# Kernel optimization log

Hardware: AMD Instinct MI355X
Metric: run time of the kernel (lower is better)

Reference implementation:

```python
import jax, jax.numpy as jnp
import numpy as np

B, S, F = 4, 2048, 512
H, DH, OUT = 8, 64, 512  # attention_dim=512 -> head_dim=64
NEG_SLOPE = 0.01


def setup_inputs() -> dict:
    key = jax.random.key(0)
    ks = jax.random.split(key, 9)
    sc_in = 1.0 / np.sqrt(F)
    sc_hd = 1.0 / np.sqrt(H * DH)
    return {
        "x": jax.random.normal(ks[0], (B, S, F), dtype=jnp.float32),
        "Wq": jax.random.normal(ks[1], (F, H, DH), dtype=jnp.float32) * sc_in,
        "bq": jnp.zeros((H, DH), dtype=jnp.float32),
        "Wk": jax.random.normal(ks[2], (F, H, DH), dtype=jnp.float32) * sc_in,
        "bk": jnp.zeros((H, DH), dtype=jnp.float32),
        "Wv": jax.random.normal(ks[3], (F, H, DH), dtype=jnp.float32) * sc_in,
        "bv": jnp.zeros((H, DH), dtype=jnp.float32),
        "Wo": jax.random.normal(ks[4], (H, DH, OUT), dtype=jnp.float32) * sc_hd,
        "bo": jnp.zeros((OUT,), dtype=jnp.float32),
    }


def reference(x, Wq, bq, Wk, bk, Wv, bv, Wo, bo):
    # QKV projections: DenseGeneral(axis=-1, features=(H, DH)) -> [B, S, H, DH]
    q = jnp.einsum('bsf,fhd->bshd', x, Wq) + bq
    k = jnp.einsum('bsf,fhd->bshd', x, Wk) + bk
    v = jnp.einsum('bsf,fhd->bshd', x, Wv) + bv

    # Pairwise squared L2: l2[b,h,i,j] = ||q[b,i,h]-k[b,j,h]||^2
    q2 = jnp.sum(q * q, axis=-1)              # [B, S, H]
    k2 = jnp.sum(k * k, axis=-1)              # [B, S, H]
    qk = jnp.einsum('bihd,bjhd->bhij', q, k)  # [B, H, S, S]
    l2 = (q2.transpose(0, 2, 1)[:, :, :, None]
          + k2.transpose(0, 2, 1)[:, :, None, :]
          - 2.0 * qk)

    # softmax over key axis j, then weights.T @ value (note the transpose:
    # output token index is j, summed over query index i, as in the original)
    w = jax.nn.softmax(-l2, axis=-1)                  # [B, H, Si, Sj]
    attn = jnp.einsum('bhij,bihd->bjhd', w, v)        # [B, S, H, DH]

    # out DenseGeneral contracting (H, DH)
    out = jnp.einsum('bshd,hdo->bso', attn, Wo) + bo
    return jnp.where(out >= 0, out, NEG_SLOPE * out)
```

## Files before the change

kernel.cpp:

```cpp
#include <hip/hip_runtime.h>


typedef __attribute__((ext_vector_type(8))) short bf16x8;
typedef __attribute__((ext_vector_type(4))) float f32x4;
typedef __attribute__((ext_vector_type(4))) unsigned short u16x4;

#define MFMA16 __builtin_amdgcn_mfma_f32_16x16x32_bf16
#define LOG2E 1.4426950408889634f
#define TWO_LOG2E 2.8853900817779268f

__device__ inline unsigned short f2bf(float f) {
  unsigned int u = __float_as_uint(f);
  unsigned int r = 0x7fffu + ((u >> 16) & 1u);
  return (unsigned short)((u + r) >> 16);
}
__device__ inline float bf2f(unsigned short h) {
  return __uint_as_float(((unsigned int)h) << 16);
}
__device__ inline float fexp2(float x) { return __builtin_amdgcn_exp2f(x); }

__device__ inline void gl_lds16(const unsigned short* g, unsigned short* lds) {
  __builtin_amdgcn_global_load_lds(
      (const __attribute__((address_space(1))) unsigned int*)g,
      (__attribute__((address_space(3))) unsigned int*)lds, 16, 0, 0);
}

#define NXB4 (8192*512/4)
#define NWQ (1536*512)
#define NWO (512*512)

__global__ __launch_bounds__(256) void prep(
    const float* __restrict__ x, const float* __restrict__ Wq,
    const float* __restrict__ Wk, const float* __restrict__ Wv,
    const float* __restrict__ Wo, const float* __restrict__ bq,
    const float* __restrict__ bk, const float* __restrict__ bv,
    unsigned short* __restrict__ xb, unsigned short* __restrict__ wqkvT,
    unsigned short* __restrict__ woT, float* __restrict__ biasp) {
  int i = blockIdx.x * blockDim.x + threadIdx.x;
  if (i < NXB4) {
    f32x4 v = ((const f32x4*)x)[i];
    u16x4 o;
    o.x = f2bf(v.x); o.y = f2bf(v.y); o.z = f2bf(v.z); o.w = f2bf(v.w);
    ((u16x4*)xb)[i] = o;
    return;
  }
  i -= NXB4;
  if (i < NWQ) {
    int n = i >> 9, f = i & 511;
    const float* W = (n < 512) ? Wq : (n < 1024) ? Wk : Wv;
    wqkvT[i] = f2bf(W[f * 512 + (n & 511)]);
    return;
  }
  i -= NWQ;
  if (i < NWO) {
    int o = i >> 9, hd = i & 511;
    woT[i] = f2bf(Wo[hd * 512 + o]);
    return;
  }
  i -= NWO;
  if (i < 1536) {
    biasp[i] = (i < 512) ? bq[i] : (i < 1024) ? bk[i - 512] : bv[i - 1024];
  }
}

template<int MODE>
__global__ __launch_bounds__(256) void gemm_bt(
    const unsigned short* __restrict__ A, const unsigned short* __restrict__ Bt,
    const float* __restrict__ bias,
    unsigned short* __restrict__ o_q, unsigned short* __restrict__ o_k,
    unsigned short* __restrict__ o_v, float* __restrict__ o_f, int K) {
  const int m0 = blockIdx.y * 128;
  const int n0 = blockIdx.x * 128;
  const int tid = threadIdx.x;
  const int w = tid >> 6, l = tid & 63, lg = l >> 4, ll = l & 15;
  const int wr = w >> 1, wc = w & 1;
  __shared__ unsigned short a_lds[128 * 32];
  __shared__ unsigned short b_lds[128 * 32];
  f32x4 acc[4][4] = {};
  const int nkt = K >> 5;
  for (int kt = 0; kt < nkt; ++kt) {
#pragma unroll
    for (int c = 0; c < 2; ++c) {
      const int cc_base = c * 256 + w * 64;
      const int cc = cc_base + l;
      const int row = cc >> 2, cl = cc & 3;
      gl_lds16(A + (size_t)(m0 + row) * K + kt * 32 + cl * 8, a_lds + cc_base * 8);
      gl_lds16(Bt + (size_t)(n0 + row) * K + kt * 32 + cl * 8, b_lds + cc_base * 8);
    }
    __syncthreads();
    bf16x8 af[4], bfr[4];
#pragma unroll
    for (int mi = 0; mi < 4; ++mi)
      af[mi] = *(const bf16x8*)(a_lds + (wr * 64 + mi * 16 + ll) * 32 + lg * 8);
#pragma unroll
    for (int ni = 0; ni < 4; ++ni)
      bfr[ni] = *(const bf16x8*)(b_lds + (wc * 64 + ni * 16 + ll) * 32 + lg * 8);
#pragma unroll
    for (int mi = 0; mi < 4; ++mi)
#pragma unroll
      for (int ni = 0; ni < 4; ++ni)
        acc[mi][ni] = MFMA16(af[mi], bfr[ni], acc[mi][ni], 0, 0, 0);
    __syncthreads();
  }
#pragma unroll
  for (int mi = 0; mi < 4; ++mi)
#pragma unroll
    for (int ni = 0; ni < 4; ++ni) {
      const int col = n0 + wc * 64 + ni * 16 + ll;
      const float bb = bias[col];
#pragma unroll
      for (int r = 0; r < 4; ++r) {
        const int row = m0 + wr * 64 + mi * 16 + lg * 4 + r;
        float v = acc[mi][ni][r] + bb;
        if (MODE == 0) {
          const int which = col >> 9, h = (col >> 6) & 7, d = col & 63;
          const int b = row >> 11, s = row & 2047;
          if (which == 0) v *= TWO_LOG2E;
          const size_t idx = ((size_t)((b * 8 + h) * 2048 + s)) * 64 + d;
          (which == 0 ? o_q : which == 1 ? o_k : o_v)[idx] = f2bf(v);
        } else {
          v = v >= 0.f ? v : 0.01f * v;
          o_f[(size_t)row * 512 + col] = v;
        }
      }
    }
}

__global__ __launch_bounds__(256) void k2_kernel(const unsigned short* __restrict__ k_g,
                                                 float* __restrict__ k2l_g) {
  const int lane = threadIdx.x & 63;
  const int wid = (blockIdx.x * blockDim.x + threadIdx.x) >> 6;
  const int nw = (gridDim.x * blockDim.x) >> 6;
  for (int row = wid; row < 32 * 2048; row += nw) {
    float v = bf2f(k_g[(size_t)row * 64 + lane]);
    v *= v;
#pragma unroll
    for (int m = 1; m < 64; m <<= 1) v += __shfl_xor(v, m);
    if (lane == 0) k2l_g[row] = LOG2E * v;
  }
}

__global__ __launch_bounds__(256) void transpose_v(const unsigned short* __restrict__ v_g,
                                                   const float* __restrict__ invl_g,
                                                   unsigned short* __restrict__ vt_g) {
  const int bh = blockIdx.x >> 5, st = blockIdx.x & 31;
  const int s0 = st * 64;
  __shared__ unsigned short tile[64][72];
  const int t = threadIdx.x;
  {
    const int sl = t >> 2, cg = t & 3;
    const float sc = invl_g[bh * 2048 + s0 + sl];
    const unsigned short* src = v_g + ((size_t)(bh * 2048 + s0 + sl)) * 64 + cg * 16;
    bf16x8 v0 = *(const bf16x8*)(src);
    bf16x8 v1 = *(const bf16x8*)(src + 8);
#pragma unroll
    for (int e = 0; e < 8; ++e) tile[sl][cg * 16 + e] = f2bf(sc * bf2f((unsigned short)v0[e]));
#pragma unroll
    for (int e = 0; e < 8; ++e) tile[sl][cg * 16 + 8 + e] = f2bf(sc * bf2f((unsigned short)v1[e]));
  }
  __syncthreads();
  {
    const int dl = t >> 2, sg = t & 3;
    bf16x8 o0, o1;
#pragma unroll
    for (int e = 0; e < 8; ++e) o0[e] = (short)tile[sg * 16 + e][dl];
#pragma unroll
    for (int e = 0; e < 8; ++e) o1[e] = (short)tile[sg * 16 + 8 + e][dl];
    unsigned short* dst = vt_g + ((size_t)(bh * 64 + dl)) * 2048 + s0 + sg * 16;
    *(bf16x8*)dst = o0;
    *(bf16x8*)(dst + 8) = o1;
  }
}

__global__ __launch_bounds__(256) void pass1(const unsigned short* __restrict__ q_g,
                                             const unsigned short* __restrict__ k_g,
                                             const float* __restrict__ k2l_g,
                                             float* __restrict__ invl_g) {
  const int bx = blockIdx.x;
  const int bh = (bx & 7) * 4 + ((bx >> 3) >> 4);
  const int ib = (bx >> 3) & 15;
  const int i0 = ib * 128;
  const int tid = threadIdx.x, w = tid >> 6, l = tid & 63, lg = l >> 4, ll = l & 15;
  __shared__ unsigned short k_lds[64 * 64];
  __shared__ float k2_lds[64];
  const unsigned short* qrow = q_g + ((size_t)(bh * 2048 + i0 + w * 32 + ll)) * 64;
  const bf16x8 qa00 = *(const bf16x8*)(qrow + lg * 8);
  const bf16x8 qa01 = *(const bf16x8*)(qrow + 32 + lg * 8);
  const bf16x8 qa10 = *(const bf16x8*)(qrow + 1024 + lg * 8);
  const bf16x8 qa11 = *(const bf16x8*)(qrow + 1024 + 32 + lg * 8);
  float lrun0[4] = {0.f, 0.f, 0.f, 0.f};
  float lrun1[4] = {0.f, 0.f, 0.f, 0.f};
  for (int jt = 0; jt < 32; ++jt) {
    const int j0 = jt * 64;
#pragma unroll
    for (int c = 0; c < 2; ++c) {
      const int cc_base = c * 256 + w * 64;
      const int cc = cc_base + l;
      const int row = cc >> 3, cl = cc & 7;
      gl_lds16(k_g + ((size_t)(bh * 2048 + j0 + row)) * 64 + ((cl ^ (row & 7)) * 8),
               k_lds + cc_base * 8);
    }
    if (tid < 64) k2_lds[tid] = k2l_g[bh * 2048 + j0 + tid];
    __syncthreads();
#pragma unroll
    for (int nf = 0; nf < 4; ++nf) {
      const int jr = nf * 16 + ll;
      const unsigned short* kb = k_lds + jr * 64;
      const int sw = jr & 7;
      bf16x8 b0 = *(const bf16x8*)(kb + ((lg ^ sw) * 8));
      bf16x8 b1 = *(const bf16x8*)(kb + (((4 + lg) ^ sw) * 8));
      f32x4 sa0 = {};
      sa0 = MFMA16(qa00, b0, sa0, 0, 0, 0);
      sa0 = MFMA16(qa01, b1, sa0, 0, 0, 0);
      f32x4 sa1 = {};
      sa1 = MFMA16(qa10, b0, sa1, 0, 0, 0);
      sa1 = MFMA16(qa11, b1, sa1, 0, 0, 0);
      const float k2v = k2_lds[jr];
      lrun0[0] += fexp2(sa0[0] - k2v);
      lrun0[1] += fexp2(sa0[1] - k2v);
      lrun0[2] += fexp2(sa0[2] - k2v);
      lrun0[3] += fexp2(sa0[3] - k2v);
      lrun1[0] += fexp2(sa1[0] - k2v);
      lrun1[1] += fexp2(sa1[1] - k2v);
      lrun1[2] += fexp2(sa1[2] - k2v);
      lrun1[3] += fexp2(sa1[3] - k2v);
    }
    __syncthreads();
  }
#pragma unroll
  for (int r = 0; r < 4; ++r) {
    float t0 = lrun0[r], t1 = lrun1[r];
#pragma unroll
    for (int m = 1; m < 16; m <<= 1) { t0 += __shfl_xor(t0, m); t1 += __shfl_xor(t1, m); }
    if (ll == 0) {
      invl_g[bh * 2048 + i0 + w * 32 + lg * 4 + r] = 1.f / t0;
      invl_g[bh * 2048 + i0 + w * 32 + 16 + lg * 4 + r] = 1.f / t1;
    }
  }
}

__global__ __launch_bounds__(256) void pass2(const unsigned short* __restrict__ q_g,
                                             const unsigned short* __restrict__ k_g,
                                             const unsigned short* __restrict__ vt_g,
                                             const float* __restrict__ k2l_g,
                                             unsigned short* __restrict__ part0,
                                             unsigned short* __restrict__ part1,
                                             unsigned short* __restrict__ part2) {
  const int bx = blockIdx.x;
  const int bh = (bx & 7) * 4 + ((bx >> 3) >> 4);
  const int jb = (bx >> 3) & 15;
  const int by = blockIdx.y;
  const int j0 = jb * 128;
  const int it0 = by * 11;
  const int it_end = (by == 2) ? 32 : it0 + 11;
  const int tid = threadIdx.x, w = tid >> 6, l = tid & 63, lg = l >> 4, ll = l & 15;
  __shared__ unsigned short q_lds[2][64 * 64];
  __shared__ unsigned short vt_lds[2][64 * 64];
  __shared__ unsigned short p_lds[128 * 64];
  const unsigned short* q_base = q_g + (size_t)bh * 2048 * 64;
  const unsigned short* vt_base = vt_g + (size_t)bh * 64 * 2048;
  const unsigned short* krow = k_g + ((size_t)(bh * 2048 + j0 + w * 32 + ll)) * 64;
  const bf16x8 ka00 = *(const bf16x8*)(krow + lg * 8);
  const bf16x8 ka01 = *(const bf16x8*)(krow + 32 + lg * 8);
  const bf16x8 ka10 = *(const bf16x8*)(krow + 1024 + lg * 8);
  const bf16x8 ka11 = *(const bf16x8*)(krow + 1024 + 32 + lg * 8);
  float k2v0[4], k2v1[4];
#pragma unroll
  for (int r = 0; r < 4; ++r) {
    k2v0[r] = k2l_g[bh * 2048 + j0 + w * 32 + lg * 4 + r];
    k2v1[r] = k2l_g[bh * 2048 + j0 + w * 32 + 16 + lg * 4 + r];
  }
  f32x4 oacc0[4] = {};
  f32x4 oacc1[4] = {};
  const int pslot = it0 & 1;
#pragma unroll
  for (int c = 0; c < 2; ++c) {
    const int cc_base = c * 256 + w * 64;
    const int cc = cc_base + l;
    const int row = cc >> 3, cl = cc & 7;
    const int csw = (cl ^ (row & 7)) * 8;
    gl_lds16(q_base + (size_t)(it0 * 64 + row) * 64 + csw, &q_lds[pslot][cc_base * 8]);
    gl_lds16(vt_base + (size_t)row * 2048 + it0 * 64 + csw, &vt_lds[pslot][cc_base * 8]);
  }
  __syncthreads();
  for (int it = it0; it < it_end; ++it) {
    const int slot = it & 1;
    if (it + 1 < it_end) {
      const int i1 = (it + 1) * 64;
#pragma unroll
      for (int c = 0; c < 2; ++c) {
        const int cc_base = c * 256 + w * 64;
        const int cc = cc_base + l;
        const int row = cc >> 3, cl = cc & 7;
        const int csw = (cl ^ (row & 7)) * 8;
        gl_lds16(q_base + (size_t)(i1 + row) * 64 + csw, &q_lds[slot ^ 1][cc_base * 8]);
        gl_lds16(vt_base + (size_t)row * 2048 + i1 + csw, &vt_lds[slot ^ 1][cc_base * 8]);
      }
    }
#pragma unroll
    for (int nf = 0; nf < 4; ++nf) {
      const int ir = nf * 16 + ll;
      const unsigned short* qb = &q_lds[slot][ir * 64];
      const int sw = ir & 7;
      bf16x8 b0 = *(const bf16x8*)(qb + ((lg ^ sw) * 8));
      bf16x8 b1 = *(const bf16x8*)(qb + (((4 + lg) ^ sw) * 8));
      f32x4 sa0 = {};
      sa0 = MFMA16(ka00, b0, sa0, 0, 0, 0);
      sa0 = MFMA16(ka01, b1, sa0, 0, 0, 0);
      f32x4 sa1 = {};
      sa1 = MFMA16(ka10, b0, sa1, 0, 0, 0);
      sa1 = MFMA16(ka11, b1, sa1, 0, 0, 0);
#pragma unroll
      for (int r = 0; r < 4; ++r) {
        const float p0 = fexp2(sa0[r] - k2v0[r]);
        const float p1 = fexp2(sa1[r] - k2v1[r]);
        const int ja = w * 32 + lg * 4 + r;
        const int jb2 = ja + 16;
        p_lds[ja * 64 + (ir ^ ((ja & 7) << 3))] =
            (unsigned short)(__float_as_uint(p0) >> 16);
        p_lds[jb2 * 64 + (ir ^ ((jb2 & 7) << 3))] =
            (unsigned short)(__float_as_uint(p1) >> 16);
      }
    }
    {
      const int jr0 = w * 32 + ll;
      const int jr1 = jr0 + 16;
      const int swp = ll & 7;
      const unsigned short* pb0 = p_lds + jr0 * 64;
      const unsigned short* pb1 = p_lds + jr1 * 64;
      bf16x8 pa00 = *(const bf16x8*)(pb0 + ((lg ^ swp) * 8));
      bf16x8 pa01 = *(const bf16x8*)(pb0 + (((4 + lg) ^ swp) * 8));
      bf16x8 pa10 = *(const bf16x8*)(pb1 + ((lg ^ swp) * 8));
      bf16x8 pa11 = *(const bf16x8*)(pb1 + (((4 + lg) ^ swp) * 8));
#pragma unroll
      for (int nf = 0; nf < 4; ++nf) {
        const int dr = nf * 16 + ll;
        const unsigned short* vb = &vt_lds[slot][dr * 64];
        const int sw = dr & 7;
        bf16x8 v0 = *(const bf16x8*)(vb + ((lg ^ sw) * 8));
        bf16x8 v1 = *(const bf16x8*)(vb + (((4 + lg) ^ sw) * 8));
        oacc0[nf] = MFMA16(pa00, v0, oacc0[nf], 0, 0, 0);
        oacc0[nf] = MFMA16(pa01, v1, oacc0[nf], 0, 0, 0);
        oacc1[nf] = MFMA16(pa10, v0, oacc1[nf], 0, 0, 0);
        oacc1[nf] = MFMA16(pa11, v1, oacc1[nf], 0, 0, 0);
      }
    }
    __syncthreads();
  }
  unsigned short* po = (by == 0) ? part0 : (by == 1) ? part1 : part2;
  const int b = bh >> 3, h2 = bh & 7;
#pragma unroll
  for (int nf = 0; nf < 4; ++nf) {
    const int d = nf * 16 + ll;
#pragma unroll
    for (int r = 0; r < 4; ++r) {
      const int j = j0 + w * 32 + lg * 4 + r;
      po[((size_t)(b * 2048 + j)) * 512 + h2 * 64 + d] = f2bf(oacc0[nf][r]);
      po[((size_t)(b * 2048 + j + 16)) * 512 + h2 * 64 + d] = f2bf(oacc1[nf][r]);
    }
  }
}

__global__ __launch_bounds__(256) void combine3(unsigned short* __restrict__ p0,
                                                const unsigned short* __restrict__ p1,
                                                const unsigned short* __restrict__ p2) {
  const int i = blockIdx.x * blockDim.x + threadIdx.x;
  bf16x8 a = ((const bf16x8*)p0)[i];
  bf16x8 b = ((const bf16x8*)p1)[i];
  bf16x8 c = ((const bf16x8*)p2)[i];
  bf16x8 o;
#pragma unroll
  for (int e = 0; e < 8; ++e)
    o[e] = (short)f2bf(bf2f((unsigned short)a[e]) + bf2f((unsigned short)b[e]) +
                       bf2f((unsigned short)c[e]));
  ((bf16x8*)p0)[i] = o;
}

extern "C" void kernel_launch(void* const* d_in, const int* in_sizes, int n_in,
                              void* d_out, int out_size, void* d_ws, size_t ws_size,
                              hipStream_t stream) {
  const float* x  = (const float*)d_in[0];
  const float* Wq = (const float*)d_in[1];
  const float* bq = (const float*)d_in[2];
  const float* Wk = (const float*)d_in[3];
  const float* bk = (const float*)d_in[4];
  const float* Wv = (const float*)d_in[5];
  const float* bv = (const float*)d_in[6];
  const float* Wo = (const float*)d_in[7];
  const float* bo = (const float*)d_in[8];
  float* out = (float*)d_out;
  char* ws = (char*)d_ws;

  unsigned short* xb    = (unsigned short*)(ws);
  unsigned short* wqkvT = (unsigned short*)(ws + 8388608);
  unsigned short* woT   = (unsigned short*)(ws + 9961472);
  float*          biasp = (float*)         (ws + 10485760);
  unsigned short* q_g   = (unsigned short*)(ws + 10493952);
  unsigned short* k_g   = (unsigned short*)(ws + 18882560);
  unsigned short* v_g   = (unsigned short*)(ws + 27271168);
  unsigned short* vt_g  = (unsigned short*)(ws + 35659776);
  float*          k2_g  = (float*)         (ws + 44048384);
  float*          invl_g= (float*)         (ws + 44310528);
  unsigned short* attnb = (unsigned short*)(ws + 44572672);
  if (ws_size < (size_t)52961280) return;

  prep<<<8199, 256, 0, stream>>>(x, Wq, Wk, Wv, Wo, bq, bk, bv, xb, wqkvT, woT, biasp);
  gemm_bt<0><<<dim3(12, 64), 256, 0, stream>>>(xb, wqkvT, biasp, q_g, k_g, v_g, nullptr, 512);
  k2_kernel<<<1024, 256, 0, stream>>>(k_g, k2_g);
  pass1<<<512, 256, 0, stream>>>(q_g, k_g, k2_g, invl_g);
  transpose_v<<<1024, 256, 0, stream>>>(v_g, invl_g, vt_g);
  pass2<<<dim3(512, 3), 256, 0, stream>>>(q_g, k_g, vt_g, k2_g, attnb, xb, v_g);
  combine3<<<2048, 256, 0, stream>>>(attnb, xb, v_g);
  gemm_bt<1><<<dim3(4, 64), 256, 0, stream>>>(attnb, woT, bo, nullptr, nullptr, nullptr, out, 512);
}
```

Baseline: 159.3 us.

## Tile weight transposes, remap GEMM block order, double-buffer K in pass1

Weight transpose-and-convert moves out of the elementwise prep kernel into a separate packW kernel that transposes through a padded 64x65 shared-memory tile, so both reads and writes are coalesced. The GEMM maps its linear block id with a stride-8 permutation, which changes which output tiles run together, likely to improve L2 reuse. Pass1 double-buffers the K tile and k2 values in LDS so the next tile's loads are issued while the current tile computes. The costs are one extra kernel launch and twice the LDS in pass1.

```diff
diff --git a/kernel.cpp b/kernel.cpp
--- a/kernel.cpp
+++ b/kernel.cpp
@@ -26,16 +26,11 @@
 }
 
 #define NXB4 (8192*512/4)
-#define NWQ (1536*512)
-#define NWO (512*512)
 
 __global__ __launch_bounds__(256) void prep(
-    const float* __restrict__ x, const float* __restrict__ Wq,
-    const float* __restrict__ Wk, const float* __restrict__ Wv,
-    const float* __restrict__ Wo, const float* __restrict__ bq,
+    const float* __restrict__ x, const float* __restrict__ bq,
     const float* __restrict__ bk, const float* __restrict__ bv,
-    unsigned short* __restrict__ xb, unsigned short* __restrict__ wqkvT,
-    unsigned short* __restrict__ woT, float* __restrict__ biasp) {
+    unsigned short* __restrict__ xb, float* __restrict__ biasp) {
   int i = blockIdx.x * blockDim.x + threadIdx.x;
   if (i < NXB4) {
     f32x4 v = ((const f32x4*)x)[i];
@@ -45,21 +40,36 @@
     return;
   }
   i -= NXB4;
-  if (i < NWQ) {
-    int n = i >> 9, f = i & 511;
-    const float* W = (n < 512) ? Wq : (n < 1024) ? Wk : Wv;
-    wqkvT[i] = f2bf(W[f * 512 + (n & 511)]);
-    return;
-  }
-  i -= NWQ;
-  if (i < NWO) {
-    int o = i >> 9, hd = i & 511;
-    woT[i] = f2bf(Wo[hd * 512 + o]);
-    return;
-  }
-  i -= NWO;
   if (i < 1536) {
     biasp[i] = (i < 512) ? bq[i] : (i < 1024) ? bk[i - 512] : bv[i - 1024];
+  }
+}
+
+__global__ __launch_bounds__(256) void packW(
+    const float* __restrict__ Wq, const float* __restrict__ Wk,
+    const float* __restrict__ Wv, const float* __restrict__ Wo,
+    unsigned short* __restrict__ wqkvT, unsigned short* __restrict__ woT) {
+  const int m = blockIdx.x >> 6;
+  const int n0 = ((blockIdx.x >> 3) & 7) * 64;
+  const int f0 = (blockIdx.x & 7) * 64;
+  const float* W = (m == 0) ? Wq : (m == 1) ? Wk : (m == 2) ? Wv : Wo;
+  __shared__ float tile[64][65];
+  const int t = threadIdx.x;
+  const int c = t & 63, r4 = t >> 6;
+#pragma unroll
+  for (int k = 0; k < 16; ++k) {
+    const int r = r4 + k * 4;
+    tile[r][c] = W[(size_t)(f0 + r) * 512 + n0 + c];
+  }
+  __syncthreads();
+#pragma unroll
+  for (int k = 0; k < 16; ++k) {
+    const int n_idx = r4 + k * 4, f_idx = c;
+    const unsigned short v = f2bf(tile[f_idx][n_idx]);
+    if (m < 3)
+      wqkvT[(size_t)(m * 512 + n0 + n_idx) * 512 + f0 + f_idx] = v;
+    else
+      woT[(size_t)(n0 + n_idx) * 512 + f0 + f_idx] = v;
   }
 }
 
@@ -69,8 +79,11 @@
     const float* __restrict__ bias,
     unsigned short* __restrict__ o_q, unsigned short* __restrict__ o_k,
     unsigned short* __restrict__ o_v, float* __restrict__ o_f, int K) {
-  const int m0 = blockIdx.y * 128;
-  const int n0 = blockIdx.x * 128;
+  const int lid = blockIdx.x + blockIdx.y * gridDim.x;
+  const int tot = gridDim.x * gridDim.y;
+  const int lid2 = (lid & 7) * (tot >> 3) + (lid >> 3);
+  const int m0 = (lid2 / gridDim.x) * 128;
+  const int n0 = (lid2 % gridDim.x) * 128;
   const int tid = threadIdx.x;
   const int w = tid >> 6, l = tid & 63, lg = l >> 4, ll = l & 15;
   const int wr = w >> 1, wc = w & 1;
@@ -181,8 +194,9 @@
   const int ib = (bx >> 3) & 15;
   const int i0 = ib * 128;
   const int tid = threadIdx.x, w = tid >> 6, l = tid & 63, lg = l >> 4, ll = l & 15;
-  __shared__ unsigned short k_lds[64 * 64];
-  __shared__ float k2_lds[64];
+  __shared__ unsigned short k_lds[2][64 * 64];
+  __shared__ float k2_lds[2][64];
+  const unsigned short* k_bh = k_g + (size_t)bh * 2048 * 64;
   const unsigned short* qrow = q_g + ((size_t)(bh * 2048 + i0 + w * 32 + ll)) * 64;
   const bf16x8 qa00 = *(const bf16x8*)(qrow + lg * 8);
   const bf16x8 qa01 = *(const bf16x8*)(qrow + 32 + lg * 8);
@@ -190,22 +204,27 @@
   const bf16x8 qa11 = *(const bf16x8*)(qrow + 1024 + 32 + lg * 8);
   float lrun0[4] = {0.f, 0.f, 0.f, 0.f};
   float lrun1[4] = {0.f, 0.f, 0.f, 0.f};
+  const int cb0 = w * 64, cb1 = 256 + w * 64;
+  const int cc0 = cb0 + l, cc1 = cb1 + l;
+  const int r0_ = cc0 >> 3, c0_ = cc0 & 7, r1_ = cc1 >> 3, c1_ = cc1 & 7;
+  const int so0 = (c0_ ^ (r0_ & 7)) * 8;
+  const int so1 = (c1_ ^ (r1_ & 7)) * 8;
+  gl_lds16(k_bh + (size_t)r0_ * 64 + so0, &k_lds[0][cb0 * 8]);
+  gl_lds16(k_bh + (size_t)r1_ * 64 + so1, &k_lds[0][cb1 * 8]);
+  if (tid < 64) k2_lds[0][tid] = k2l_g[bh * 2048 + tid];
+  __syncthreads();
   for (int jt = 0; jt < 32; ++jt) {
-    const int j0 = jt * 64;
-#pragma unroll
-    for (int c = 0; c < 2; ++c) {
-      const int cc_base = c * 256 + w * 64;
-      const int cc = cc_base + l;
-      const int row = cc >> 3, cl = cc & 7;
-      gl_lds16(k_g + ((size_t)(bh * 2048 + j0 + row)) * 64 + ((cl ^ (row & 7)) * 8),
-               k_lds + cc_base * 8);
-    }
-    if (tid < 64) k2_lds[tid] = k2l_g[bh * 2048 + j0 + tid];
-    __syncthreads();
+    const int slot = jt & 1;
+    if (jt + 1 < 32) {
+      const int j1 = (jt + 1) * 64;
+      gl_lds16(k_bh + (size_t)(j1 + r0_) * 64 + so0, &k_lds[slot ^ 1][cb0 * 8]);
+      gl_lds16(k_bh + (size_t)(j1 + r1_) * 64 + so1, &k_lds[slot ^ 1][cb1 * 8]);
+      if (tid < 64) k2_lds[slot ^ 1][tid] = k2l_g[bh * 2048 + j1 + tid];
+    }
 #pragma unroll
     for (int nf = 0; nf < 4; ++nf) {
       const int jr = nf * 16 + ll;
-      const unsigned short* kb = k_lds + jr * 64;
+      const unsigned short* kb = &k_lds[slot][jr * 64];
       const int sw = jr & 7;
       bf16x8 b0 = *(const bf16x8*)(kb + ((lg ^ sw) * 8));
       bf16x8 b1 = *(const bf16x8*)(kb + (((4 + lg) ^ sw) * 8));
@@ -215,7 +234,7 @@
       f32x4 sa1 = {};
       sa1 = MFMA16(qa10, b0, sa1, 0, 0, 0);
       sa1 = MFMA16(qa11, b1, sa1, 0, 0, 0);
-      const float k2v = k2_lds[jr];
+      const float k2v = k2_lds[slot][jr];
       lrun0[0] += fexp2(sa0[0] - k2v);
       lrun0[1] += fexp2(sa0[1] - k2v);
       lrun0[2] += fexp2(sa0[2] - k2v);
@@ -404,7 +423,8 @@
   unsigned short* attnb = (unsigned short*)(ws + 44572672);
   if (ws_size < (size_t)52961280) return;
 
-  prep<<<8199, 256, 0, stream>>>(x, Wq, Wk, Wv, Wo, bq, bk, bv, xb, wqkvT, woT, biasp);
+  prep<<<4102, 256, 0, stream>>>(x, bq, bk, bv, xb, biasp);
+  packW<<<256, 256, 0, stream>>>(Wq, Wk, Wv, Wo, wqkvT, woT);
   gemm_bt<0><<<dim3(12, 64), 256, 0, stream>>>(xb, wqkvT, biasp, q_g, k_g, v_g, nullptr, 512);
   k2_kernel<<<1024, 256, 0, stream>>>(k_g, k2_g);
   pass1<<<512, 256, 0, stream>>>(q_g, k_g, k2_g, invl_g);
```

Measured after the change: 157.1 us. No clear change (-1.4%).
